# Performance work log

Measured on AMD Instinct MI355X. Metric: run time of the kernel, lower is better.

Reference implementation:

```python
import jax, jax.numpy as jnp
import numpy as np

NODES = 16384                       # power of two -> all heap levels complete
DEPTH = (NODES - 1).bit_length() + 1  # 15 heap steps, linears k = 0..14
IN_F = 64
OUT_F = 64
MINHEAP = 0
BATCH = 32


def setup_inputs() -> dict:
    key = jax.random.key(0)
    k1, k2, k3 = jax.random.split(key, 3)
    x = jax.random.normal(k1, (BATCH, NODES, IN_F), dtype=jnp.float32)
    # stacked per-heap-step Linear params, torch layout W: [out, in]
    W = jax.random.normal(k2, (DEPTH - MINHEAP, OUT_F, IN_F), dtype=jnp.float32) * 0.05
    b = jax.random.normal(k3, (DEPTH - MINHEAP, OUT_F), dtype=jnp.float32) * 0.05
    return {"x": x, "W": W, "b": b}


def reference(x, W, b):
    # HeapLinear forward. Heap layout: level l occupies nodes [2^(l-1), 2^l)
    # (root = node 0, level(j) = bit_length(j)). The original double loop over
    # (input level l, linear k) with repeat_interleave(2^k) is equivalent to:
    #   output[j] = sum_{k=minheap}^{depth-1, level(j)>=k} linears[k](input[j >> k])
    # for power-of-two `nodes` (every out block satisfies out_node1 <= nodes).
    nodes = x.shape[-2]
    depth = (nodes - 1).bit_length() + 1
    j = np.arange(nodes)
    levels = np.array([int(v).bit_length() for v in j])  # static, trace-time
    out = jnp.zeros(x.shape[:-1] + (W.shape[1],), dtype=x.dtype)
    for k in range(MINHEAP, depth):
        n_anc = max(nodes >> k, 1)  # only nodes 0..n_anc-1 serve as distance-k ancestors
        # small per-level Linear applied to ancestor slice: [..., n_anc, out]
        t = jnp.einsum('...ni,oi->...no', x[..., :n_anc, :], W[k - MINHEAP]) + b[k - MINHEAP]
        anc = j >> k                      # distance-k ancestor of each node
        mask = levels >= k                # nodes shallower than k have no such ancestor
        out = out + jnp.where(mask[:, None], t[..., anc, :], jnp.zeros((), x.dtype))
    return out
```

## Files before the change

kernel.cpp:

```cpp
#include <hip/hip_runtime.h>

#define NODES 16384
#define NF 64
#define NBLK 128
#define TROW 72
#define BATCH 32

#define WS_WBF_OFF   0ull
#define WS_WT_OFF    122880ull
#define WS_BPRE_OFF  368640ull
#define WS_FAR_OFF   372480ull
#define WS_NEEDED    1421056ull

typedef __attribute__((ext_vector_type(8))) short short8;
typedef __attribute__((ext_vector_type(4))) short shortx4;
typedef __attribute__((ext_vector_type(4))) float floatx4;

__device__ __forceinline__ short f2bf(float f) {
    unsigned u = __float_as_uint(f);
    u += 0x7fffu + ((u >> 16) & 1u);
    return (short)(u >> 16);
}
__device__ __forceinline__ float bf2f(short s) {
    return __uint_as_float(((unsigned)(unsigned short)s) << 16);
}
__device__ __forceinline__ short8 cvt8(floatx4 a, floatx4 c) {
    short8 r;
    r[0]=f2bf(a[0]); r[1]=f2bf(a[1]); r[2]=f2bf(a[2]); r[3]=f2bf(a[3]);
    r[4]=f2bf(c[0]); r[5]=f2bf(c[1]); r[6]=f2bf(c[2]); r[7]=f2bf(c[3]);
    return r;
}

__global__ __launch_bounds__(256)
void heaplin_prep1(const float* __restrict__ W, const float* __restrict__ bias,
                   short* __restrict__ wbf, float* __restrict__ wt,
                   float* __restrict__ bpre)
{
    const int blk = blockIdx.x;
    const int tid = threadIdx.x;
    if (blk < 30) {
        int e = blk * 2048 + tid * 8;
        floatx4 a = *(const floatx4*)(W + e);
        floatx4 c = *(const floatx4*)(W + e + 4);
        *(short8*)(wbf + e) = cvt8(a, c);
    } else if (blk == 30) {
        if (tid < 64) {
            float run = 0.f;
            for (int k = 0; k < 15; ++k) { run += bias[k * 64 + tid]; bpre[k * 64 + tid] = run; }
        }
    } else {
        int k = blk - 31;
        #pragma unroll
        for (int it = 0; it < 16; ++it) {
            int idx = tid + it * 256;
            int o = idx >> 6, i = idx & 63;
            wt[k * 4096 + i * 64 + o] = W[k * 4096 + idx];
        }
    }
}

__global__ __launch_bounds__(256)
void heaplin_prep2(const float* __restrict__ x, const float* __restrict__ wt,
                   const float* __restrict__ bpre, float* __restrict__ far)
{
    __shared__ float xl[64 * 64];
    __shared__ float Zl[127 * 64];
    const int tid = threadIdx.x;
    const int b   = blockIdx.x;
    const float* xb = x + (size_t)b * NODES * NF;

    #pragma unroll
    for (int i = 0; i < 4; ++i) {
        int job = tid + i * 256;
        *(floatx4*)(xl + job * 4) = *(const floatx4*)(xb + job * 4);
    }
    __syncthreads();

    const int wave = tid >> 6, lane = tid & 63;
    const int o4 = lane & 15, j = lane >> 4;
    for (int r = wave; r < 127; r += 4) {
        int t, a;
        if (r < 64)       { t = 1; a = r; }
        else if (r < 96)  { t = 2; a = r - 64; }
        else if (r < 112) { t = 3; a = r - 96; }
        else if (r < 120) { t = 4; a = r - 112; }
        else if (r < 124) { t = 5; a = r - 120; }
        else if (r < 126) { t = 6; a = r - 124; }
        else              { t = 7; a = 0; }
        const float* wtk = wt + (7 + t) * 4096;
        floatx4 acc = {0.f, 0.f, 0.f, 0.f};
        #pragma unroll
        for (int i16 = 0; i16 < 16; ++i16) {
            int i = j + i16 * 4;
            floatx4 w4 = *(const floatx4*)(wtk + i * 64 + o4 * 4);
            float xs = xl[a * 64 + i];
            acc[0] += w4[0]*xs; acc[1] += w4[1]*xs; acc[2] += w4[2]*xs; acc[3] += w4[3]*xs;
        }
        #pragma unroll
        for (int c = 0; c < 4; ++c) {
            acc[c] += __shfl_xor(acc[c], 16, 64);
            acc[c] += __shfl_xor(acc[c], 32, 64);
        }
        if (j == 0) *(floatx4*)(Zl + r * 64 + o4 * 4) = acc;
    }
    __syncthreads();

    for (int it = 0; it < 32; ++it) {
        int job = tid + it * 256;
        if (job < 127 * 64) {
            int m = 1 + (job >> 6), o = job & 63;
            int bl = 32 - __clz(m);
            float s = bpre[(7 + bl) * 64 + o];
            #pragma unroll
            for (int t = 1; t <= 7; ++t)
                if (t <= bl) s += Zl[(128 - (128 >> (t - 1)) + (m >> t)) * 64 + o];
            far[((size_t)b * 128 + m) * 64 + o] = s;
        }
    }
}

__global__ __launch_bounds__(256, 2)
void heaplin_main(const float* __restrict__ x, const short* __restrict__ wbf,
                  const float* __restrict__ far, const float* __restrict__ bpre,
                  float* __restrict__ out)
{
    __shared__ short tbuf[128 * TROW];

    const int tid  = threadIdx.x;
    const int lane = tid & 63;
    const int wave = tid >> 6;
    const int lr = lane & 15;
    const int lq = lane >> 4;
    const int nblk = blockIdx.x;
    const int b    = blockIdx.y;
    const float* xb = x + (size_t)b * NODES * NF;
    float* ob = out + (size_t)b * NODES * NF;
    const floatx4 zero4 = {0.f, 0.f, 0.f, 0.f};

    if (nblk == 0) {
        floatx4 accE[8];
        #pragma unroll
        for (int t8 = 0; t8 < 8; ++t8) accE[t8] = zero4;

        for (int k = 0; k < 8; ++k) {
            __syncthreads();
            #pragma unroll
            for (int i = 0; i < 8; ++i) {
                int job = tid + i * 256;
                int r = job >> 4, c4 = job & 15;
                bool valid = (k == 0) || (r >= (1 << (k - 1)));
                floatx4 vv = zero4;
                if (valid) vv = *(const floatx4*)(xb + (r >> k) * NF + c4 * 4);
                shortx4 s4;
                s4[0]=f2bf(vv[0]); s4[1]=f2bf(vv[1]); s4[2]=f2bf(vv[2]); s4[3]=f2bf(vv[3]);
                *(shortx4*)(tbuf + r * TROW + c4 * 4) = s4;
            }
            __syncthreads();
            #pragma unroll
            for (int t8 = 0; t8 < 8; ++t8) {
                int mt = 2 * wave + (t8 & 1);
                int nt = t8 >> 1;
                int arow = mt * 16 + lr;
                const short* wp = wbf + k * 4096 + (nt * 16 + lr) * 64 + lq * 8;
                short8 b0 = *(const short8*)wp;
                short8 b1 = *(const short8*)(wp + 32);
                short8 a0 = *(const short8*)(tbuf + arow * TROW + lq * 8);
                short8 a1 = *(const short8*)(tbuf + arow * TROW + 32 + lq * 8);
                accE[t8] = __builtin_amdgcn_mfma_f32_16x16x32_bf16(a0, b0, accE[t8], 0, 0, 0);
                accE[t8] = __builtin_amdgcn_mfma_f32_16x16x32_bf16(a1, b1, accE[t8], 0, 0, 0);
            }
        }
        #pragma unroll
        for (int t8 = 0; t8 < 8; ++t8) {
            int mt = 2 * wave + (t8 & 1);
            int nt = t8 >> 1;
            int c = nt * 16 + lr;
            #pragma unroll
            for (int rg = 0; rg < 4; ++rg) {
                int j = mt * 16 + lq * 4 + rg;
                int lvl = (j == 0) ? 0 : (32 - __clz(j));
                ob[(size_t)j * NF + c] = accE[t8][rg] + bpre[lvl * 64 + c];
            }
        }
        return;
    }

    const int n0 = nblk * NBLK;

    #pragma unroll
    for (int g = 0; g < 3; ++g) {
        const int idx = wave + g * 4;
        const bool gvalid = (idx < 11);
        const int idxc = gvalid ? idx : 0;
        int k, mt;
        if (idxc < 4)       { k = 1; mt = idxc; }
        else if (idxc < 6)  { k = 2; mt = idxc - 4; }
        else if (idxc == 6) { k = 3; mt = 0; }
        else                { k = idxc - 3; mt = 0; }
        const int anc = n0 >> k;
        const int rowb = (anc & ~15) + mt * 16;
        const float* ap = xb + (size_t)(rowb + lr) * NF + lq * 8;
        floatx4 f0 = *(const floatx4*)ap,        f1 = *(const floatx4*)(ap + 4);
        floatx4 f2 = *(const floatx4*)(ap + 32), f3 = *(const floatx4*)(ap + 36);
        short8 a0 = cvt8(f0, f1), a1 = cvt8(f2, f3);
        const int tb  = 128 - (256 >> k);
        const int cnt = 128 >> k;
        const int off = anc & 15;
        #pragma unroll
        for (int nt = 0; nt < 4; ++nt) {
            const short* wp = wbf + k * 4096 + (nt * 16 + lr) * 64 + lq * 8;
            short8 b0 = *(const short8*)wp;
            short8 b1 = *(const short8*)(wp + 32);
            floatx4 acc = zero4;
            acc = __builtin_amdgcn_mfma_f32_16x16x32_bf16(a0, b0, acc, 0, 0, 0);
            acc = __builtin_amdgcn_mfma_f32_16x16x32_bf16(a1, b1, acc, 0, 0, 0);
            if (gvalid) {
                #pragma unroll
                for (int rg = 0; rg < 4; ++rg) {
                    int m = lq * 4 + rg;
                    if (k <= 3) {
                        tbuf[(tb + mt * 16 + m) * TROW + nt * 16 + lr] = f2bf(acc[rg]);
                    } else if (m >= off && m < off + cnt) {
                        tbuf[(tb + m - off) * TROW + nt * 16 + lr] = f2bf(acc[rg]);
                    }
                }
            }
        }
    }

    floatx4 accE[8];
    {
        const float* apA = xb + (size_t)(n0 + 2 * wave * 16 + lr) * NF + lq * 8;
        const float* apB = apA + 16 * NF;
        floatx4 fA0 = *(const floatx4*)apA,        fA1 = *(const floatx4*)(apA + 4);
        floatx4 fA2 = *(const floatx4*)(apA + 32), fA3 = *(const floatx4*)(apA + 36);
        floatx4 fB0 = *(const floatx4*)apB,        fB1 = *(const floatx4*)(apB + 4);
        floatx4 fB2 = *(const floatx4*)(apB + 32), fB3 = *(const floatx4*)(apB + 36);
        short8 aA0 = cvt8(fA0, fA1), aA1 = cvt8(fA2, fA3);
        short8 aB0 = cvt8(fB0, fB1), aB1 = cvt8(fB2, fB3);
        #pragma unroll
        for (int nt = 0; nt < 4; ++nt) {
            const short* wp = wbf + (nt * 16 + lr) * 64 + lq * 8;
            short8 b0 = *(const short8*)wp;
            short8 b1 = *(const short8*)(wp + 32);
            floatx4 accA = zero4, accB = zero4;
            accA = __builtin_amdgcn_mfma_f32_16x16x32_bf16(aA0, b0, accA, 0, 0, 0);
            accA = __builtin_amdgcn_mfma_f32_16x16x32_bf16(aA1, b1, accA, 0, 0, 0);
            accB = __builtin_amdgcn_mfma_f32_16x16x32_bf16(aB0, b0, accB, 0, 0, 0);
            accB = __builtin_amdgcn_mfma_f32_16x16x32_bf16(aB1, b1, accB, 0, 0, 0);
            accE[2 * nt + 0] = accA;
            accE[2 * nt + 1] = accB;
        }
    }

    const int mD  = tid >> 2;
    const int c0D = (tid & 3) * 16;
    floatx4 fvv[4];
    {
        const float* fv = far + ((size_t)b * 128 + nblk) * 64 + c0D;
        #pragma unroll
        for (int i = 0; i < 4; ++i) fvv[i] = *(const floatx4*)(fv + i * 4);
    }
    __syncthreads();

    {
        float e[16];
        #pragma unroll
        for (int i = 0; i < 16; ++i) {
            int c = c0D + i;
            e[i] = bf2f(tbuf[ mD               * TROW + c])
                 + bf2f(tbuf[(64  + (mD >> 1)) * TROW + c])
                 + bf2f(tbuf[(96  + (mD >> 2)) * TROW + c])
                 + bf2f(tbuf[(112 + (mD >> 3)) * TROW + c])
                 + bf2f(tbuf[(120 + (mD >> 4)) * TROW + c])
                 + bf2f(tbuf[(124 + (mD >> 5)) * TROW + c])
                 + bf2f(tbuf[126               * TROW + c])
                 + fvv[i >> 2][i & 3];
        }
        __syncthreads();
        #pragma unroll
        for (int i = 0; i < 16; ++i) tbuf[mD * TROW + c0D + i] = f2bf(e[i]);
    }
    __syncthreads();

    #pragma unroll
    for (int t8 = 0; t8 < 8; ++t8) {
        int mt = 2 * wave + (t8 & 1);
        int nt = t8 >> 1;
        int c = nt * 16 + lr;
        #pragma unroll
        for (int rg = 0; rg < 4; ++rg) {
            int j = mt * 16 + lq * 4 + rg;
            float val = accE[t8][rg] + bf2f(tbuf[(j >> 1) * TROW + c]);
            ob[(size_t)(n0 + j) * NF + c] = val;
        }
    }
}

#define SROW 72
#define SROWS 270
__global__ __launch_bounds__(256, 4)
void heaplin_fallback(const float* __restrict__ x, const float* __restrict__ W,
                      const float* __restrict__ bias, float* __restrict__ out)
{
    __shared__ short stage[SROWS * SROW];
    __shared__ float farpart[4 * 64];
    short* tbuf = stage;
    float* cumB = (float*)(stage + 128 * SROW);

    const int tid  = threadIdx.x;
    const int lane = tid & 63;
    const int wave = tid >> 6;
    const int lr = lane & 15;
    const int lq = lane >> 4;
    const int nblk = blockIdx.x;
    const int b    = blockIdx.y;
    const float* xb = x + (size_t)b * NODES * NF;
    float* ob = out + (size_t)b * NODES * NF;
    const floatx4 zero4 = {0.f, 0.f, 0.f, 0.f};

    if (nblk == 0) {
        if (tid < 64) {
            float run = 0.f;
            for (int k = 0; k < 15; ++k) { run += bias[k * 64 + tid]; cumB[k * 64 + tid] = run; }
        }
        floatx4 accE[8];
        #pragma unroll
        for (int t8 = 0; t8 < 8; ++t8) accE[t8] = zero4;
        for (int k = 0; k < 8; ++k) {
            __syncthreads();
            #pragma unroll
            for (int i = 0; i < 8; ++i) {
                int job = tid + i * 256;
                int r = job >> 4, c4 = job & 15;
                bool valid = (k == 0) || (r >= (1 << (k - 1)));
                floatx4 vv = zero4;
                if (valid) vv = *(const floatx4*)(xb + (r >> k) * NF + c4 * 4);
                shortx4 s4;
                s4[0]=f2bf(vv[0]); s4[1]=f2bf(vv[1]); s4[2]=f2bf(vv[2]); s4[3]=f2bf(vv[3]);
                *(shortx4*)(stage + r * SROW + c4 * 4) = s4;
            }
            __syncthreads();
            #pragma unroll
            for (int t8 = 0; t8 < 8; ++t8) {
                int mt = 2 * wave + (t8 & 1);
                int nt = t8 >> 1;
                int arow = mt * 16 + lr;
                const float* wr = W + k * 4096 + (nt * 16 + lr) * 64 + lq * 8;
                floatx4 wa = *(const floatx4*)wr, wb2 = *(const floatx4*)(wr + 4);
                short8 b0 = cvt8(wa, wb2);
                floatx4 wc = *(const floatx4*)(wr + 32), wd = *(const floatx4*)(wr + 36);
                short8 b1 = cvt8(wc, wd);
                short8 a0 = *(const short8*)(stage + arow * SROW + lq * 8);
                short8 a1 = *(const short8*)(stage + arow * SROW + 32 + lq * 8);
                accE[t8] = __builtin_amdgcn_mfma_f32_16x16x32_bf16(a0, b0, accE[t8], 0, 0, 0);
                accE[t8] = __builtin_amdgcn_mfma_f32_16x16x32_bf16(a1, b1, accE[t8], 0, 0, 0);
            }
        }
        #pragma unroll
        for (int t8 = 0; t8 < 8; ++t8) {
            int mt = 2 * wave + (t8 & 1);
            int nt = t8 >> 1;
            int c = nt * 16 + lr;
            #pragma unroll
            for (int rg = 0; rg < 4; ++rg) {
                int j = mt * 16 + lq * 4 + rg;
                int lvl = (j == 0) ? 0 : (32 - __clz(j));
                ob[(size_t)j * NF + c] = accE[t8][rg] + cumB[lvl * 64 + c];
            }
        }
        return;
    }

    const int n0 = nblk * NBLK;
    const int L  = 32 - __clz(n0);
    floatx4 v[16];
    #pragma unroll
    for (int i = 0; i < 16; ++i) {
        int job = tid + i * 256;
        int r = job >> 4, c4 = job & 15;
        int node;
        if (r < 128)        node = n0 + r;
        else if (r >= 254)  node = n0 >> 7;
        else { int k = __clz(255 - r) - 24; node = (n0 >> k) + r - (256 - (256 >> k)); }
        v[i] = *(const floatx4*)(xb + (size_t)node * NF + c4 * 4);
    }
    #pragma unroll
    for (int i = 0; i < 16; ++i) {
        int job = tid + i * 256;
        int r = job >> 4, c4 = job & 15;
        shortx4 s4;
        s4[0]=f2bf(v[i][0]); s4[1]=f2bf(v[i][1]); s4[2]=f2bf(v[i][2]); s4[3]=f2bf(v[i][3]);
        *(shortx4*)(stage + r * SROW + c4 * 4) = s4;
    }
    __syncthreads();
    floatx4 accE[8];
    #pragma unroll
    for (int t8 = 0; t8 < 8; ++t8) {
        int mt = 2 * wave + (t8 & 1);
        int nt = t8 >> 1;
        int arow = mt * 16 + lr;
        const float* wr = W + (nt * 16 + lr) * 64 + lq * 8;
        floatx4 wa = *(const floatx4*)wr, wb2 = *(const floatx4*)(wr + 4);
        short8 b0 = cvt8(wa, wb2);
        floatx4 wc = *(const floatx4*)(wr + 32), wd = *(const floatx4*)(wr + 36);
        short8 b1 = cvt8(wc, wd);
        short8 a0 = *(const short8*)(stage + arow * SROW + lq * 8);
        short8 a1 = *(const short8*)(stage + arow * SROW + 32 + lq * 8);
        floatx4 acc = zero4;
        acc = __builtin_amdgcn_mfma_f32_16x16x32_bf16(a0, b0, acc, 0, 0, 0);
        acc = __builtin_amdgcn_mfma_f32_16x16x32_bf16(a1, b1, acc, 0, 0, 0);
        accE[t8] = acc;
    }
    {
        float p = 0.f;
        const int q = wave, o = lane;
        for (int k = 8; k <= L; ++k) {
            const float* xa = xb + (size_t)(n0 >> k) * NF + q * 16;
            const float* wr = W + k * 4096 + o * 64 + q * 16;
            #pragma unroll
            for (int i = 0; i < 4; ++i) {
                floatx4 wv = *(const floatx4*)(wr + i * 4);
                floatx4 xv = *(const floatx4*)(xa + i * 4);
                p += wv[0]*xv[0] + wv[1]*xv[1] + wv[2]*xv[2] + wv[3]*xv[3];
            }
        }
        if (q == 0) for (int k = 0; k <= L; ++k) p += bias[k * 64 + o];
        farpart[q * 64 + o] = p;
    }
    __syncthreads();
    for (int jj = 0; jj < 11; ++jj) {
        int job = wave + jj * 4;
        int idx = job % 11;
        int nt  = job / 11;
        int k, mt;
        if (idx < 4)      { k = 1; mt = idx; }
        else if (idx < 6) { k = 2; mt = idx - 4; }
        else if (idx < 7) { k = 3; mt = 0; }
        else              { k = idx - 3; mt = 0; }
        int sbase = 256 - (256 >> k);
        int arow = sbase + mt * 16 + lr;
        const float* wr = W + k * 4096 + (nt * 16 + lr) * 64 + lq * 8;
        floatx4 wa = *(const floatx4*)wr, wb2 = *(const floatx4*)(wr + 4);
        short8 b0 = cvt8(wa, wb2);
        floatx4 wc = *(const floatx4*)(wr + 32), wd = *(const floatx4*)(wr + 36);
        short8 b1 = cvt8(wc, wd);
        short8 a0 = *(const short8*)(stage + arow * SROW + lq * 8);
        short8 a1 = *(const short8*)(stage + arow * SROW + 32 + lq * 8);
        floatx4 acc = zero4;
        acc = __builtin_amdgcn_mfma_f32_16x16x32_bf16(a0, b0, acc, 0, 0, 0);
        acc = __builtin_amdgcn_mfma_f32_16x16x32_bf16(a1, b1, acc, 0, 0, 0);
        int tb = 128 - (256 >> k);
        int nvalid = 128 >> k;
        #pragma unroll
        for (int rg = 0; rg < 4; ++rg) {
            int m = mt * 16 + lq * 4 + rg;
            if (m < nvalid) tbuf[(tb + m) * TROW + nt * 16 + lr] = f2bf(acc[rg]);
        }
    }
    __syncthreads();
    {
        int m  = tid >> 2;
        int c0 = (tid & 3) * 16;
        float e[16];
        #pragma unroll
        for (int i = 0; i < 16; ++i) {
            int c = c0 + i;
            e[i] = bf2f(tbuf[ m               * TROW + c])
                 + bf2f(tbuf[(64  + (m >> 1)) * TROW + c])
                 + bf2f(tbuf[(96  + (m >> 2)) * TROW + c])
                 + bf2f(tbuf[(112 + (m >> 3)) * TROW + c])
                 + bf2f(tbuf[(120 + (m >> 4)) * TROW + c])
                 + bf2f(tbuf[(124 + (m >> 5)) * TROW + c])
                 + bf2f(tbuf[126              * TROW + c])
                 + farpart[c] + farpart[64 + c] + farpart[128 + c] + farpart[192 + c];
        }
        #pragma unroll
        for (int i = 0; i < 16; ++i) tbuf[m * TROW + c0 + i] = f2bf(e[i]);
    }
    __syncthreads();
    #pragma unroll
    for (int t8 = 0; t8 < 8; ++t8) {
        int mt = 2 * wave + (t8 & 1);
        int nt = t8 >> 1;
        int c = nt * 16 + lr;
        #pragma unroll
        for (int rg = 0; rg < 4; ++rg) {
            int j = mt * 16 + lq * 4 + rg;
            float val = accE[t8][rg] + bf2f(tbuf[(j >> 1) * TROW + c]);
            ob[(size_t)(n0 + j) * NF + c] = val;
        }
    }
}

extern "C" void kernel_launch(void* const* d_in, const int* in_sizes, int n_in,
                              void* d_out, int out_size, void* d_ws, size_t ws_size,
                              hipStream_t stream) {
    const float* x  = (const float*)d_in[0];
    const float* W  = (const float*)d_in[1];
    const float* bs = (const float*)d_in[2];
    float* out = (float*)d_out;
    dim3 grid(NODES / NBLK, BATCH);
    if (ws_size >= WS_NEEDED) {
        short* wbf  = (short*)((char*)d_ws + WS_WBF_OFF);
        float* wt   = (float*)((char*)d_ws + WS_WT_OFF);
        float* bpre = (float*)((char*)d_ws + WS_BPRE_OFF);
        float* farb = (float*)((char*)d_ws + WS_FAR_OFF);
        heaplin_prep1<<<46, 256, 0, stream>>>(W, bs, wbf, wt, bpre);
        heaplin_prep2<<<32, 256, 0, stream>>>(x, wt, bpre, farb);
        heaplin_main<<<grid, 256, 0, stream>>>(x, wbf, farb, bpre, out);
    } else {
        heaplin_fallback<<<grid, 256, 0, stream>>>(x, W, bs, out);
    }
}
```

Measured before the change: 332.3 us.

## Swap MFMA operands to transpose accumulators and vectorize stores and LDS reads

Result: slower. 344.0 us (+3.5%).

```diff
diff --git a/kernel.cpp b/kernel.cpp
--- a/kernel.cpp
+++ b/kernel.cpp
@@ -166,26 +166,43 @@
                 short8 b1 = *(const short8*)(wp + 32);
                 short8 a0 = *(const short8*)(tbuf + arow * TROW + lq * 8);
                 short8 a1 = *(const short8*)(tbuf + arow * TROW + 32 + lq * 8);
-                accE[t8] = __builtin_amdgcn_mfma_f32_16x16x32_bf16(a0, b0, accE[t8], 0, 0, 0);
-                accE[t8] = __builtin_amdgcn_mfma_f32_16x16x32_bf16(a1, b1, accE[t8], 0, 0, 0);
+                accE[t8] = __builtin_amdgcn_mfma_f32_16x16x32_bf16(b0, a0, accE[t8], 0, 0, 0);
+                accE[t8] = __builtin_amdgcn_mfma_f32_16x16x32_bf16(b1, a1, accE[t8], 0, 0, 0);
             }
         }
         #pragma unroll
         for (int t8 = 0; t8 < 8; ++t8) {
             int mt = 2 * wave + (t8 & 1);
             int nt = t8 >> 1;
-            int c = nt * 16 + lr;
-            #pragma unroll
-            for (int rg = 0; rg < 4; ++rg) {
-                int j = mt * 16 + lq * 4 + rg;
-                int lvl = (j == 0) ? 0 : (32 - __clz(j));
-                ob[(size_t)j * NF + c] = accE[t8][rg] + bpre[lvl * 64 + c];
-            }
+            int j  = mt * 16 + lr;
+            int c4 = nt * 16 + lq * 4;
+            int lvl = (j == 0) ? 0 : (32 - __clz(j));
+            floatx4 bp = *(const floatx4*)(bpre + lvl * 64 + c4);
+            floatx4 v;
+            #pragma unroll
+            for (int rg = 0; rg < 4; ++rg) v[rg] = accE[t8][rg] + bp[rg];
+            *(floatx4*)(ob + (size_t)j * NF + c4) = v;
         }
         return;
     }
 
     const int n0 = nblk * NBLK;
+
+    const float* apA = xb + (size_t)(n0 + 2 * wave * 16 + lr) * NF + lq * 8;
+    const float* apB = apA + 16 * NF;
+    floatx4 fA0 = *(const floatx4*)apA,        fA1 = *(const floatx4*)(apA + 4);
+    floatx4 fA2 = *(const floatx4*)(apA + 32), fA3 = *(const floatx4*)(apA + 36);
+    floatx4 fB0 = *(const floatx4*)apB,        fB1 = *(const floatx4*)(apB + 4);
+    floatx4 fB2 = *(const floatx4*)(apB + 32), fB3 = *(const floatx4*)(apB + 36);
+
+    const int mD  = tid >> 2;
+    const int c0D = (tid & 3) * 16;
+    floatx4 fvv[4];
+    {
+        const float* fv = far + ((size_t)b * 128 + nblk) * 64 + c0D;
+        #pragma unroll
+        for (int i = 0; i < 4; ++i) fvv[i] = *(const floatx4*)(fv + i * 4);
+    }
 
     #pragma unroll
     for (int g = 0; g < 3; ++g) {
@@ -206,36 +223,27 @@
         const int tb  = 128 - (256 >> k);
         const int cnt = 128 >> k;
         const int off = anc & 15;
+        int row; bool rvalid;
+        if (k <= 3) { row = tb + mt * 16 + lr; rvalid = true; }
+        else        { row = tb + lr - off;     rvalid = (lr >= off) && (lr < off + cnt); }
         #pragma unroll
         for (int nt = 0; nt < 4; ++nt) {
             const short* wp = wbf + k * 4096 + (nt * 16 + lr) * 64 + lq * 8;
             short8 b0 = *(const short8*)wp;
             short8 b1 = *(const short8*)(wp + 32);
             floatx4 acc = zero4;
-            acc = __builtin_amdgcn_mfma_f32_16x16x32_bf16(a0, b0, acc, 0, 0, 0);
-            acc = __builtin_amdgcn_mfma_f32_16x16x32_bf16(a1, b1, acc, 0, 0, 0);
-            if (gvalid) {
-                #pragma unroll
-                for (int rg = 0; rg < 4; ++rg) {
-                    int m = lq * 4 + rg;
-                    if (k <= 3) {
-                        tbuf[(tb + mt * 16 + m) * TROW + nt * 16 + lr] = f2bf(acc[rg]);
-                    } else if (m >= off && m < off + cnt) {
-                        tbuf[(tb + m - off) * TROW + nt * 16 + lr] = f2bf(acc[rg]);
-                    }
-                }
+            acc = __builtin_amdgcn_mfma_f32_16x16x32_bf16(b0, a0, acc, 0, 0, 0);
+            acc = __builtin_amdgcn_mfma_f32_16x16x32_bf16(b1, a1, acc, 0, 0, 0);
+            if (gvalid && rvalid) {
+                shortx4 s4;
+                s4[0]=f2bf(acc[0]); s4[1]=f2bf(acc[1]); s4[2]=f2bf(acc[2]); s4[3]=f2bf(acc[3]);
+                *(shortx4*)(tbuf + row * TROW + nt * 16 + lq * 4) = s4;
             }
         }
     }
 
     floatx4 accE[8];
     {
-        const float* apA = xb + (size_t)(n0 + 2 * wave * 16 + lr) * NF + lq * 8;
-        const float* apB = apA + 16 * NF;
-        floatx4 fA0 = *(const floatx4*)apA,        fA1 = *(const floatx4*)(apA + 4);
-        floatx4 fA2 = *(const floatx4*)(apA + 32), fA3 = *(const floatx4*)(apA + 36);
-        floatx4 fB0 = *(const floatx4*)apB,        fB1 = *(const floatx4*)(apB + 4);
-        floatx4 fB2 = *(const floatx4*)(apB + 32), fB3 = *(const floatx4*)(apB + 36);
         short8 aA0 = cvt8(fA0, fA1), aA1 = cvt8(fA2, fA3);
         short8 aB0 = cvt8(fB0, fB1), aB1 = cvt8(fB2, fB3);
         #pragma unroll
@@ -244,42 +252,45 @@
             short8 b0 = *(const short8*)wp;
             short8 b1 = *(const short8*)(wp + 32);
             floatx4 accA = zero4, accB = zero4;
-            accA = __builtin_amdgcn_mfma_f32_16x16x32_bf16(aA0, b0, accA, 0, 0, 0);
-            accA = __builtin_amdgcn_mfma_f32_16x16x32_bf16(aA1, b1, accA, 0, 0, 0);
-            accB = __builtin_amdgcn_mfma_f32_16x16x32_bf16(aB0, b0, accB, 0, 0, 0);
-            accB = __builtin_amdgcn_mfma_f32_16x16x32_bf16(aB1, b1, accB, 0, 0, 0);
+            accA = __builtin_amdgcn_mfma_f32_16x16x32_bf16(b0, aA0, accA, 0, 0, 0);
+            accA = __builtin_amdgcn_mfma_f32_16x16x32_bf16(b1, aA1, accA, 0, 0, 0);
+            accB = __builtin_amdgcn_mfma_f32_16x16x32_bf16(b0, aB0, accB, 0, 0, 0);
+            accB = __builtin_amdgcn_mfma_f32_16x16x32_bf16(b1, aB1, accB, 0, 0, 0);
             accE[2 * nt + 0] = accA;
             accE[2 * nt + 1] = accB;
         }
     }
-
-    const int mD  = tid >> 2;
-    const int c0D = (tid & 3) * 16;
-    floatx4 fvv[4];
+    __syncthreads();
+
     {
-        const float* fv = far + ((size_t)b * 128 + nblk) * 64 + c0D;
-        #pragma unroll
-        for (int i = 0; i < 4; ++i) fvv[i] = *(const floatx4*)(fv + i * 4);
-    }
-    __syncthreads();
-
-    {
+        const short* tb0 = tbuf + mD                * TROW + c0D;
+        const short* tb1 = tbuf + (64  + (mD >> 1)) * TROW + c0D;
+        const short* tb2 = tbuf + (96  + (mD >> 2)) * TROW + c0D;
+        const short* tb3 = tbuf + (112 + (mD >> 3)) * TROW + c0D;
+        const short* tb4 = tbuf + (120 + (mD >> 4)) * TROW + c0D;
+        const short* tb5 = tbuf + (124 + (mD >> 5)) * TROW + c0D;
+        const short* tb6 = tbuf + 126               * TROW + c0D;
+        short8 r0a = *(const short8*)tb0, r0b = *(const short8*)(tb0 + 8);
+        short8 r1a = *(const short8*)tb1, r1b = *(const short8*)(tb1 + 8);
+        short8 r2a = *(const short8*)tb2, r2b = *(const short8*)(tb2 + 8);
+        short8 r3a = *(const short8*)tb3, r3b = *(const short8*)(tb3 + 8);
+        short8 r4a = *(const short8*)tb4, r4b = *(const short8*)(tb4 + 8);
+        short8 r5a = *(const short8*)tb5, r5b = *(const short8*)(tb5 + 8);
+        short8 r6a = *(const short8*)tb6, r6b = *(const short8*)(tb6 + 8);
         float e[16];
         #pragma unroll
-        for (int i = 0; i < 16; ++i) {
-            int c = c0D + i;
-            e[i] = bf2f(tbuf[ mD               * TROW + c])
-                 + bf2f(tbuf[(64  + (mD >> 1)) * TROW + c])
-                 + bf2f(tbuf[(96  + (mD >> 2)) * TROW + c])
-                 + bf2f(tbuf[(112 + (mD >> 3)) * TROW + c])
-                 + bf2f(tbuf[(120 + (mD >> 4)) * TROW + c])
-                 + bf2f(tbuf[(124 + (mD >> 5)) * TROW + c])
-                 + bf2f(tbuf[126               * TROW + c])
-                 + fvv[i >> 2][i & 3];
+        for (int i = 0; i < 8; ++i) {
+            e[i]     = bf2f(r0a[i]) + bf2f(r1a[i]) + bf2f(r2a[i]) + bf2f(r3a[i])
+                     + bf2f(r4a[i]) + bf2f(r5a[i]) + bf2f(r6a[i]) + fvv[i >> 2][i & 3];
+            e[i + 8] = bf2f(r0b[i]) + bf2f(r1b[i]) + bf2f(r2b[i]) + bf2f(r3b[i])
+                     + bf2f(r4b[i]) + bf2f(r5b[i]) + bf2f(r6b[i]) + fvv[(i + 8) >> 2][i & 3];
         }
         __syncthreads();
-        #pragma unroll
-        for (int i = 0; i < 16; ++i) tbuf[mD * TROW + c0D + i] = f2bf(e[i]);
+        short8 wlo, whi;
+        #pragma unroll
+        for (int i = 0; i < 8; ++i) { wlo[i] = f2bf(e[i]); whi[i] = f2bf(e[i + 8]); }
+        *(short8*)(tbuf + mD * TROW + c0D)     = wlo;
+        *(short8*)(tbuf + mD * TROW + c0D + 8) = whi;
     }
     __syncthreads();
 
@@ -287,13 +298,13 @@
     for (int t8 = 0; t8 < 8; ++t8) {
         int mt = 2 * wave + (t8 & 1);
         int nt = t8 >> 1;
-        int c = nt * 16 + lr;
-        #pragma unroll
-        for (int rg = 0; rg < 4; ++rg) {
-            int j = mt * 16 + lq * 4 + rg;
-            float val = accE[t8][rg] + bf2f(tbuf[(j >> 1) * TROW + c]);
-            ob[(size_t)(n0 + j) * NF + c] = val;
-        }
+        int j  = mt * 16 + lr;
+        int c4 = nt * 16 + lq * 4;
+        shortx4 u = *(const shortx4*)(tbuf + (mt * 8 + (lr >> 1)) * TROW + c4);
+        floatx4 v;
+        #pragma unroll
+        for (int rg = 0; rg < 4; ++rg) v[rg] = accE[t8][rg] + bf2f(u[rg]);
+        *(floatx4*)(ob + (size_t)(n0 + j) * NF + c4) = v;
     }
 }
 
```
